# Performance work log

Hardware: AMD Instinct MI355X
Metric: run time of the kernel (lower is better)

Reference implementation:

```python
import jax, jax.numpy as jnp
import numpy as np

N = 20000       # nodes
E = 160000      # edges (avg degree 8)
NFEAT = 512
NHID = 512
NCLASS = 64
NLAYERS = 4


def setup_inputs() -> dict:
    key = jax.random.key(0)
    ks = jax.random.split(key, 9)
    s = 0.05
    x = jax.random.normal(ks[0], (N, NFEAT), dtype=jnp.float32)
    edge_index = jax.random.randint(ks[1], (2, E), 0, N, dtype=jnp.int64)
    W_enc = jax.random.normal(ks[2], (NFEAT, NHID), dtype=jnp.float32) * s
    b_enc = jnp.zeros((NHID,), dtype=jnp.float32)
    W_convs = jax.random.normal(ks[3], (NLAYERS, NHID, NHID), dtype=jnp.float32) * s
    b_convs = jnp.zeros((NLAYERS, NHID), dtype=jnp.float32)
    W_dec = jax.random.normal(ks[4], (NHID, NCLASS), dtype=jnp.float32) * s
    b_dec = jnp.zeros((NCLASS,), dtype=jnp.float32)
    return {"x": x, "edge_index": edge_index, "W_enc": W_enc, "b_enc": b_enc,
            "W_convs": W_convs, "b_convs": b_convs, "W_dec": W_dec, "b_dec": b_dec}


def reference(x, edge_index, W_enc, b_enc, W_convs, b_convs, W_dec, b_dec):
    n = x.shape[0]
    loops = jnp.arange(n, dtype=edge_index.dtype)
    # GCNConv adds self-loops, then sym-normalizes: D^-1/2 (A+I) D^-1/2
    src = jnp.concatenate([edge_index[0], loops])  # [E+N]
    dst = jnp.concatenate([edge_index[1], loops])  # [E+N]
    deg = jax.ops.segment_sum(jnp.ones_like(dst, dtype=x.dtype), dst, num_segments=N)
    dinv = jnp.where(deg > 0, jax.lax.rsqrt(deg), jnp.zeros_like(deg))
    norm = (dinv[src] * dinv[dst])[:, None]  # [E+N, 1]

    # encoder: relu(Linear)
    h = jax.nn.relu(x @ W_enc + b_enc)

    def gcn_step(h, wb):
        W, b = wb
        hW = h @ W                                   # [N, H]
        msg = hW[src] * norm                         # gather + scale
        agg = jax.ops.segment_sum(msg, dst, num_segments=N)  # scatter-add
        return jax.nn.relu(agg + b), None            # bias after aggregation (PyG)

    h, _ = jax.lax.scan(gcn_step, h, (W_convs, b_convs))

    # decoder (dropout p=0 in eval -> identity)
    return h @ W_dec + b_dec
```

## Files before the change

kernel.cpp:

```cpp
#include <hip/hip_runtime.h>

#define N_NODES 20000
#define E_EDGES 160000
#define NFEAT   512
#define NHID    512
#define NCLASS  64
#define NLAYERS 4

#define SCAN_CHUNK 1024
#define NBLK ((N_NODES + SCAN_CHUNK - 1) / SCAN_CHUNK)

using bf16x8 = __attribute__((ext_vector_type(8))) short;
using f32x4  = __attribute__((ext_vector_type(4))) float;
using u16x8  = __attribute__((ext_vector_type(8))) unsigned short;

__device__ __forceinline__ unsigned short f2bf(float f) {
    union { float f; unsigned int u; } v; v.f = f;
    unsigned int u = v.u + 0x7FFFu + ((v.u >> 16) & 1u);
    return (unsigned short)(u >> 16);
}
__device__ __forceinline__ float bf2f(unsigned short h) {
    union { unsigned int u; float f; } v; v.u = ((unsigned int)h) << 16;
    return v.f;
}
__device__ __forceinline__ void gl2lds16(const void* gptr, void* lptr) {
    __builtin_amdgcn_global_load_lds(
        (const __attribute__((address_space(1))) unsigned int*)gptr,
        (__attribute__((address_space(3))) unsigned int*)lptr,
        16, 0, 0);
}


__global__ __launch_bounds__(256) void conv_f32_bf16(const float* __restrict__ in,
                                                     unsigned short* __restrict__ out,
                                                     int n4) {
    int i = blockIdx.x * 256 + threadIdx.x;
    if (i < n4) {
        float4 v = ((const float4*)in)[i];
        ushort4 o;
        o.x = f2bf(v.x); o.y = f2bf(v.y); o.z = f2bf(v.z); o.w = f2bf(v.w);
        ((ushort4*)out)[i] = o;
    }
}

__global__ __launch_bounds__(256) void transpose_bf16(const float* __restrict__ W,
                                                      unsigned short* __restrict__ WT,
                                                      int K, int N) {
    __shared__ float tile[32][33];
    const int k0 = blockIdx.y * 32, n0 = blockIdx.x * 32;
    const int tx = threadIdx.x & 31, ty = threadIdx.x >> 5;
#pragma unroll
    for (int i = 0; i < 32; i += 8)
        tile[ty + i][tx] = W[(size_t)(k0 + ty + i) * N + n0 + tx];
    __syncthreads();
#pragma unroll
    for (int i = 0; i < 32; i += 8)
        WT[(size_t)(n0 + ty + i) * K + k0 + tx] = f2bf(tile[tx][ty + i]);
}

__global__ __launch_bounds__(256) void csr_count(const int* __restrict__ dst,
                                                 int* __restrict__ counts) {
    int e = blockIdx.x * 256 + threadIdx.x;
    if (e < E_EDGES) atomicAdd(&counts[dst[e]], 1);
}

__global__ __launch_bounds__(256) void block_sums(const int* __restrict__ counts,
                                                  int* __restrict__ bsums) {
    __shared__ int red[256];
    const int b = blockIdx.x, t = threadIdx.x;
    const int base = b * SCAN_CHUNK + t * 4;
    int s = 0;
    if (base + 3 < N_NODES) {
        int4 v = *(const int4*)(counts + base);
        s = v.x + v.y + v.z + v.w;
    } else {
        for (int i = 0; i < 4; ++i)
            if (base + i < N_NODES) s += counts[base + i];
    }
    red[t] = s;
    __syncthreads();
    for (int off = 128; off > 0; off >>= 1) {
        if (t < off) red[t] += red[t + off];
        __syncthreads();
    }
    if (t == 0) bsums[b] = red[0];
}

__global__ __launch_bounds__(64) void scan_bsums(const int* __restrict__ bsums,
                                                 int* __restrict__ boffs) {
    const int t = threadIdx.x;
    const int orig = (t < NBLK) ? bsums[t] : 0;
    int v = orig;
    for (int off = 1; off < 64; off <<= 1) {
        int u = __shfl_up(v, off, 64);
        if (t >= off) v += u;
    }
    if (t < NBLK) boffs[t] = v - orig;
}

__global__ __launch_bounds__(256) void write_rowptr(const int* __restrict__ counts,
                                                    const int* __restrict__ boffs,
                                                    int* __restrict__ row_ptr) {
    __shared__ int part[256];
    const int b = blockIdx.x, t = threadIdx.x;
    const int base = b * SCAN_CHUNK + t * 4;
    int c[4], s = 0;
    for (int i = 0; i < 4; ++i) {
        int idx = base + i;
        c[i] = (idx < N_NODES) ? counts[idx] : 0;
        s += c[i];
    }
    part[t] = s;
    __syncthreads();
    for (int off = 1; off < 256; off <<= 1) {
        int v = (t >= off) ? part[t - off] : 0;
        __syncthreads();
        part[t] += v;
        __syncthreads();
    }
    int run = boffs[b] + ((t == 0) ? 0 : part[t - 1]);
    for (int i = 0; i < 4; ++i) {
        int idx = base + i;
        if (idx < N_NODES) { row_ptr[idx] = run; run += c[i]; }
    }
    if (b == 0 && t == 0) row_ptr[N_NODES] = E_EDGES;
}

__global__ __launch_bounds__(256) void node_prep(const int* __restrict__ counts,
                                                 const int* __restrict__ row_ptr,
                                                 float* __restrict__ dinv,
                                                 int* __restrict__ cursor) {
    int i = blockIdx.x * 256 + threadIdx.x;
    if (i < N_NODES) {
        dinv[i] = rsqrtf((float)counts[i] + 1.0f);
        cursor[i] = row_ptr[i];
    }
}

__global__ __launch_bounds__(256) void csr_fill(const int* __restrict__ src,
                                                const int* __restrict__ dst,
                                                const float* __restrict__ dinv,
                                                int* __restrict__ cursor,
                                                int* __restrict__ col,
                                                float* __restrict__ wgt) {
    int e = blockIdx.x * 256 + threadIdx.x;
    if (e < E_EDGES) {
        int s = src[e], d = dst[e];
        int pos = atomicAdd(&cursor[d], 1);
        col[pos] = s;
        wgt[pos] = dinv[s] * dinv[d];
    }
}

template <int BN, bool RELU, bool HASBIAS, bool OUTBF16>
__global__ __launch_bounds__(256) void gemm_mfma(const unsigned short* __restrict__ A,
                                                 const unsigned short* __restrict__ BT,
                                                 const float* __restrict__ bias,
                                                 void* __restrict__ Cout,
                                                 int M, int N, int K) {
    constexpr int BM = 128, BK = 32;
    constexpr int R = (BN == 128) ? 4 : 2;
    constexpr int C = 4;
    __shared__ unsigned short lA[BM * BK];
    __shared__ unsigned short lB[BN * BK];

    const int t    = threadIdx.x;
    const int lane = t & 63;
    const int wv   = t >> 6;
    const int wr   = (BN == 128) ? (wv >> 1) : wv;
    const int wc   = (BN == 128) ? (wv & 1) : 0;
    const int lm   = lane & 15;
    const int quad = lane >> 4;

    const int m0 = blockIdx.y * BM;
    const int n0 = blockIdx.x * BN;

    f32x4 acc[R][C] = {};

    for (int kt = 0; kt < K; kt += BK) {
#pragma unroll
        for (int i = 0; i < (BM * BK) / (256 * 8); ++i) {
            int idx = i * 256 + t;
            int row = idx >> 2;
            int kof = (idx & 3) << 3;
            int gr = m0 + row; if (gr >= M) gr = M - 1;
            gl2lds16(A + (size_t)gr * K + kt + kof, &lA[idx * 8]);
        }
#pragma unroll
        for (int i = 0; i < (BN * BK) / (256 * 8); ++i) {
            int idx = i * 256 + t;
            int row = idx >> 2;
            int kof = (idx & 3) << 3;
            gl2lds16(BT + (size_t)(n0 + row) * K + kt + kof, &lB[idx * 8]);
        }
        __syncthreads();

        bf16x8 af[R], bfr[C];
#pragma unroll
        for (int r = 0; r < R; ++r)
            af[r] = *(const bf16x8*)&lA[(wr * R * 16 + r * 16 + lm) * BK + quad * 8];
#pragma unroll
        for (int c = 0; c < C; ++c)
            bfr[c] = *(const bf16x8*)&lB[(wc * C * 16 + c * 16 + lm) * BK + quad * 8];
#pragma unroll
        for (int r = 0; r < R; ++r)
#pragma unroll
            for (int c = 0; c < C; ++c)
                acc[r][c] = __builtin_amdgcn_mfma_f32_16x16x32_bf16(af[r], bfr[c],
                                                                    acc[r][c], 0, 0, 0);
        __syncthreads();
    }

#pragma unroll
    for (int r = 0; r < R; ++r) {
#pragma unroll
        for (int c = 0; c < C; ++c) {
            const int colg = n0 + wc * C * 16 + c * 16 + lm;
            const float bb = HASBIAS ? bias[colg] : 0.0f;
            const int rowb = m0 + wr * R * 16 + r * 16 + quad * 4;
#pragma unroll
            for (int i = 0; i < 4; ++i) {
                const int rr = rowb + i;
                if (rr < M) {
                    float v = acc[r][c][i] + bb;
                    if (RELU) v = fmaxf(v, 0.0f);
                    if (OUTBF16)
                        ((unsigned short*)Cout)[(size_t)rr * N + colg] = f2bf(v);
                    else
                        ((float*)Cout)[(size_t)rr * N + colg] = v;
                }
            }
        }
    }
}

__global__ __launch_bounds__(256) void gcn_aggregate(const unsigned short* __restrict__ hW,
                                                     const int* __restrict__ row_ptr,
                                                     const int* __restrict__ col,
                                                     const float* __restrict__ wgt,
                                                     const float* __restrict__ dinv,
                                                     const float* __restrict__ bias,
                                                     unsigned short* __restrict__ out) {
    const int wv   = threadIdx.x >> 6;
    const int lane = threadIdx.x & 63;
    const int d    = blockIdx.x * 4 + wv;
    if (d >= N_NODES) return;
    const int beg = row_ptr[d];
    const int end = row_ptr[d + 1];
    const size_t foff = (size_t)lane * 8;

    const float di = dinv[d];
    const float sl = di * di;
    u16x8 sv = *(const u16x8*)(hW + (size_t)d * NHID + foff);
    float acc[8];
#pragma unroll
    for (int i = 0; i < 8; ++i) acc[i] = bf2f(sv[i]) * sl;

    for (int j = beg; j < end; ++j) {
        const int s   = col[j];
        const float w = wgt[j];
        u16x8 v = *(const u16x8*)(hW + (size_t)s * NHID + foff);
#pragma unroll
        for (int i = 0; i < 8; ++i) acc[i] += bf2f(v[i]) * w;
    }

    const float4 b0 = *(const float4*)(bias + foff);
    const float4 b1 = *(const float4*)(bias + foff + 4);
    u16x8 r;
    r[0] = f2bf(fmaxf(acc[0] + b0.x, 0.0f));
    r[1] = f2bf(fmaxf(acc[1] + b0.y, 0.0f));
    r[2] = f2bf(fmaxf(acc[2] + b0.z, 0.0f));
    r[3] = f2bf(fmaxf(acc[3] + b0.w, 0.0f));
    r[4] = f2bf(fmaxf(acc[4] + b1.x, 0.0f));
    r[5] = f2bf(fmaxf(acc[5] + b1.y, 0.0f));
    r[6] = f2bf(fmaxf(acc[6] + b1.z, 0.0f));
    r[7] = f2bf(fmaxf(acc[7] + b1.w, 0.0f));
    *(u16x8*)(out + (size_t)d * NHID + foff) = r;
}

extern "C" void kernel_launch(void* const* d_in, const int* in_sizes, int n_in,
                              void* d_out, int out_size, void* d_ws, size_t ws_size,
                              hipStream_t stream) {
    const float* x       = (const float*)d_in[0];
    const int*   ei      = (const int*)d_in[1];
    const float* W_enc   = (const float*)d_in[2];
    const float* b_enc   = (const float*)d_in[3];
    const float* W_convs = (const float*)d_in[4];
    const float* b_convs = (const float*)d_in[5];
    const float* W_dec   = (const float*)d_in[6];
    const float* b_dec   = (const float*)d_in[7];
    float* out = (float*)d_out;

    const int* src = ei;
    const int* dst = ei + E_EDGES;

    char* ws = (char*)d_ws;
    auto alloc = [&](size_t bytes) {
        char* p = ws;
        ws += (bytes + 255) / 256 * 256;
        return p;
    };
    float* dinv     = (float*)alloc(N_NODES * 4);
    int*   counts   = (int*)  alloc(N_NODES * 4);
    int*   row_ptr  = (int*)  alloc((N_NODES + 1) * 4);
    int*   cursor   = (int*)  alloc(N_NODES * 4);
    int*   bsums    = (int*)  alloc(NBLK * 4);
    int*   boffs    = (int*)  alloc(NBLK * 4);
    int*   colA     = (int*)  alloc(E_EDGES * 4);
    float* wgtA     = (float*)alloc(E_EDGES * 4);
    unsigned short* xbf   = (unsigned short*)alloc((size_t)N_NODES * NFEAT * 2);
    unsigned short* WencT = (unsigned short*)alloc((size_t)NFEAT * NHID * 2);
    unsigned short* WcvT  = (unsigned short*)alloc((size_t)NLAYERS * NHID * NHID * 2);
    unsigned short* WdecT = (unsigned short*)alloc((size_t)NHID * NCLASS * 2);
    unsigned short* B1    = (unsigned short*)alloc((size_t)N_NODES * NHID * 2);
    unsigned short* B2    = (unsigned short*)alloc((size_t)N_NODES * NHID * 2);

    hipMemsetAsync(counts, 0, N_NODES * sizeof(int), stream);
    csr_count<<<(E_EDGES + 255) / 256, 256, 0, stream>>>(dst, counts);
    block_sums<<<NBLK, 256, 0, stream>>>(counts, bsums);
    scan_bsums<<<1, 64, 0, stream>>>(bsums, boffs);
    write_rowptr<<<NBLK, 256, 0, stream>>>(counts, boffs, row_ptr);
    node_prep<<<(N_NODES + 255) / 256, 256, 0, stream>>>(counts, row_ptr, dinv, cursor);
    csr_fill<<<(E_EDGES + 255) / 256, 256, 0, stream>>>(src, dst, dinv, cursor, colA, wgtA);

    {
        int n4 = N_NODES * NFEAT / 4;
        conv_f32_bf16<<<(n4 + 255) / 256, 256, 0, stream>>>(x, xbf, n4);
    }
    transpose_bf16<<<dim3(NHID / 32, NFEAT / 32), 256, 0, stream>>>(W_enc, WencT, NFEAT, NHID);
    for (int L = 0; L < NLAYERS; ++L)
        transpose_bf16<<<dim3(NHID / 32, NHID / 32), 256, 0, stream>>>(
            W_convs + (size_t)L * NHID * NHID, WcvT + (size_t)L * NHID * NHID, NHID, NHID);
    transpose_bf16<<<dim3(NCLASS / 32, NHID / 32), 256, 0, stream>>>(W_dec, WdecT, NHID, NCLASS);

    const int MB = (N_NODES + 127) / 128;

    gemm_mfma<128, true, true, true><<<dim3(NHID / 128, MB), 256, 0, stream>>>(
        xbf, WencT, b_enc, B1, N_NODES, NHID, NFEAT);

    for (int L = 0; L < NLAYERS; ++L) {
        gemm_mfma<128, false, false, true><<<dim3(NHID / 128, MB), 256, 0, stream>>>(
            B1, WcvT + (size_t)L * NHID * NHID, nullptr, B2, N_NODES, NHID, NHID);
        gcn_aggregate<<<(N_NODES + 3) / 4, 256, 0, stream>>>(
            B2, row_ptr, colA, wgtA, dinv, b_convs + (size_t)L * NHID, B1);
    }

    gemm_mfma<64, false, true, false><<<dim3(NCLASS / 64, MB), 256, 0, stream>>>(
        B1, WdecT, b_dec, out, N_NODES, NCLASS, NHID);
}
```

Before: 399.9 us.

## Batch edge loads via wave shuffles in aggregation and merge prep kernels

Result: faster. 378.0 us (-5.5%).

```diff
diff --git a/kernel.cpp b/kernel.cpp
--- a/kernel.cpp
+++ b/kernel.cpp
@@ -43,11 +43,24 @@
     }
 }
 
-__global__ __launch_bounds__(256) void transpose_bf16(const float* __restrict__ W,
-                                                      unsigned short* __restrict__ WT,
-                                                      int K, int N) {
+__global__ __launch_bounds__(256) void transpose_all(const float* __restrict__ W_enc,
+                                                     const float* __restrict__ W_convs,
+                                                     const float* __restrict__ W_dec,
+                                                     unsigned short* __restrict__ WencT,
+                                                     unsigned short* __restrict__ WcvT,
+                                                     unsigned short* __restrict__ WdecT) {
     __shared__ float tile[32][33];
-    const int k0 = blockIdx.y * 32, n0 = blockIdx.x * 32;
+    const int id = blockIdx.z;
+    const float* W; unsigned short* WT; int N;
+    const int K = 512;
+    if (id == 0)                { W = W_enc; WT = WencT; N = NHID; }
+    else if (id <= NLAYERS)     { W = W_convs + (size_t)(id - 1) * NHID * NHID;
+                                  WT = WcvT  + (size_t)(id - 1) * NHID * NHID; N = NHID; }
+    else                        { W = W_dec; WT = WdecT; N = NCLASS; }
+
+    const int n0 = blockIdx.x * 32;
+    if (n0 >= N) return;
+    const int k0 = blockIdx.y * 32;
     const int tx = threadIdx.x & 31, ty = threadIdx.x >> 5;
 #pragma unroll
     for (int i = 0; i < 32; i += 8)
@@ -100,7 +113,9 @@
 
 __global__ __launch_bounds__(256) void write_rowptr(const int* __restrict__ counts,
                                                     const int* __restrict__ boffs,
-                                                    int* __restrict__ row_ptr) {
+                                                    int* __restrict__ row_ptr,
+                                                    int* __restrict__ cursor,
+                                                    float* __restrict__ dinv) {
     __shared__ int part[256];
     const int b = blockIdx.x, t = threadIdx.x;
     const int base = b * SCAN_CHUNK + t * 4;
@@ -121,20 +136,14 @@
     int run = boffs[b] + ((t == 0) ? 0 : part[t - 1]);
     for (int i = 0; i < 4; ++i) {
         int idx = base + i;
-        if (idx < N_NODES) { row_ptr[idx] = run; run += c[i]; }
+        if (idx < N_NODES) {
+            row_ptr[idx] = run;
+            cursor[idx]  = run;
+            dinv[idx]    = rsqrtf((float)c[i] + 1.0f);
+            run += c[i];
+        }
     }
     if (b == 0 && t == 0) row_ptr[N_NODES] = E_EDGES;
-}
-
-__global__ __launch_bounds__(256) void node_prep(const int* __restrict__ counts,
-                                                 const int* __restrict__ row_ptr,
-                                                 float* __restrict__ dinv,
-                                                 int* __restrict__ cursor) {
-    int i = blockIdx.x * 256 + threadIdx.x;
-    if (i < N_NODES) {
-        dinv[i] = rsqrtf((float)counts[i] + 1.0f);
-        cursor[i] = row_ptr[i];
-    }
 }
 
 __global__ __launch_bounds__(256) void csr_fill(const int* __restrict__ src,
@@ -256,25 +265,45 @@
 #pragma unroll
     for (int i = 0; i < 8; ++i) acc[i] = bf2f(sv[i]) * sl;
 
-    for (int j = beg; j < end; ++j) {
-        const int s   = col[j];
-        const float w = wgt[j];
-        u16x8 v = *(const u16x8*)(hW + (size_t)s * NHID + foff);
-#pragma unroll
-        for (int i = 0; i < 8; ++i) acc[i] += bf2f(v[i]) * w;
-    }
-
-    const float4 b0 = *(const float4*)(bias + foff);
-    const float4 b1 = *(const float4*)(bias + foff + 4);
+    for (int b0 = beg; b0 < end; b0 += 64) {
+        const int nb   = min(64, end - b0);
+        const int last = nb - 1;
+        int   myc = 0;
+        float myw = 0.0f;
+        if (lane < nb) { myc = col[b0 + lane]; myw = wgt[b0 + lane]; }
+
+        for (int j = 0; j < nb; j += 8) {
+            int   s[8];
+            float w[8];
+            u16x8 v[8];
+#pragma unroll
+            for (int k = 0; k < 8; ++k) {
+                const int jj = j + k;
+                s[k] = __shfl(myc, jj <= last ? jj : last);
+                w[k] = (jj <= last) ? __shfl(myw, jj) : 0.0f;
+            }
+#pragma unroll
+            for (int k = 0; k < 8; ++k)
+                v[k] = *(const u16x8*)(hW + (size_t)s[k] * NHID + foff);
+#pragma unroll
+            for (int k = 0; k < 8; ++k)
+#pragma unroll
+                for (int i = 0; i < 8; ++i)
+                    acc[i] += bf2f(v[k][i]) * w[k];
+        }
+    }
+
+    const float4 b0v = *(const float4*)(bias + foff);
+    const float4 b1v = *(const float4*)(bias + foff + 4);
     u16x8 r;
-    r[0] = f2bf(fmaxf(acc[0] + b0.x, 0.0f));
-    r[1] = f2bf(fmaxf(acc[1] + b0.y, 0.0f));
-    r[2] = f2bf(fmaxf(acc[2] + b0.z, 0.0f));
-    r[3] = f2bf(fmaxf(acc[3] + b0.w, 0.0f));
-    r[4] = f2bf(fmaxf(acc[4] + b1.x, 0.0f));
-    r[5] = f2bf(fmaxf(acc[5] + b1.y, 0.0f));
-    r[6] = f2bf(fmaxf(acc[6] + b1.z, 0.0f));
-    r[7] = f2bf(fmaxf(acc[7] + b1.w, 0.0f));
+    r[0] = f2bf(fmaxf(acc[0] + b0v.x, 0.0f));
+    r[1] = f2bf(fmaxf(acc[1] + b0v.y, 0.0f));
+    r[2] = f2bf(fmaxf(acc[2] + b0v.z, 0.0f));
+    r[3] = f2bf(fmaxf(acc[3] + b0v.w, 0.0f));
+    r[4] = f2bf(fmaxf(acc[4] + b1v.x, 0.0f));
+    r[5] = f2bf(fmaxf(acc[5] + b1v.y, 0.0f));
+    r[6] = f2bf(fmaxf(acc[6] + b1v.z, 0.0f));
+    r[7] = f2bf(fmaxf(acc[7] + b1v.w, 0.0f));
     *(u16x8*)(out + (size_t)d * NHID + foff) = r;
 }
 
@@ -319,19 +348,15 @@
     csr_count<<<(E_EDGES + 255) / 256, 256, 0, stream>>>(dst, counts);
     block_sums<<<NBLK, 256, 0, stream>>>(counts, bsums);
     scan_bsums<<<1, 64, 0, stream>>>(bsums, boffs);
-    write_rowptr<<<NBLK, 256, 0, stream>>>(counts, boffs, row_ptr);
-    node_prep<<<(N_NODES + 255) / 256, 256, 0, stream>>>(counts, row_ptr, dinv, cursor);
+    write_rowptr<<<NBLK, 256, 0, stream>>>(counts, boffs, row_ptr, cursor, dinv);
     csr_fill<<<(E_EDGES + 255) / 256, 256, 0, stream>>>(src, dst, dinv, cursor, colA, wgtA);
 
     {
         int n4 = N_NODES * NFEAT / 4;
         conv_f32_bf16<<<(n4 + 255) / 256, 256, 0, stream>>>(x, xbf, n4);
     }
-    transpose_bf16<<<dim3(NHID / 32, NFEAT / 32), 256, 0, stream>>>(W_enc, WencT, NFEAT, NHID);
-    for (int L = 0; L < NLAYERS; ++L)
-        transpose_bf16<<<dim3(NHID / 32, NHID / 32), 256, 0, stream>>>(
-            W_convs + (size_t)L * NHID * NHID, WcvT + (size_t)L * NHID * NHID, NHID, NHID);
-    transpose_bf16<<<dim3(NCLASS / 32, NHID / 32), 256, 0, stream>>>(W_dec, WdecT, NHID, NCLASS);
+    transpose_all<<<dim3(16, 16, NLAYERS + 2), 256, 0, stream>>>(
+        W_enc, W_convs, W_dec, WencT, WcvT, WdecT);
 
     const int MB = (N_NODES + 127) / 128;
 
```
